# Kernel tuning notes

Measured on AMD Instinct MI355X. Metric: run time of the kernel, lower is better.

The kernel has to match this reference:

```python
import jax, jax.numpy as jnp
import numpy as np


def setup_inputs() -> dict:
    key = jax.random.key(0)
    k1, k2, k3 = jax.random.split(key, 3)
    B, C, H, W = 64, 2048, 14, 14
    M, NC = 32, 396
    x = jax.random.normal(k1, (B, C, H, W), dtype=jnp.float32)
    Wa = jax.random.normal(k2, (M, C), dtype=jnp.float32) * (1.0 / np.sqrt(C))
    ba = jnp.zeros((M,), dtype=jnp.float32)
    Wc = jax.random.normal(k3, (NC, M * C), dtype=jnp.float32) * (1.0 / np.sqrt(M * C))
    bc = jnp.zeros((NC,), dtype=jnp.float32)
    return {"x": x, "Wa": Wa, "ba": ba, "Wc": Wc, "bc": bc}


def reference(x, Wa, ba, Wc, bc):
    # x: [B, C, H, W]
    B, C, H, W = x.shape
    M = Wa.shape[0]
    # 1x1 conv == channel contraction; attention maps [B, M, H, W]
    A = jax.nn.sigmoid(jnp.einsum('bchw,mc->bmhw', x, Wa) + ba[None, :, None, None])
    # BAP: per-head attention-weighted global average pool -> [B, M, C]
    bap = jnp.einsum('bchw,bmhw->bmc', x, A) / (H * W)
    feats = bap.reshape(B, M * C)  # concat head-major, matching torch cat order
    return feats @ Wc.T + bc
```

## Files before the change

kernel.cpp:

```cpp
#include <hip/hip_runtime.h>
#include <hip/hip_bf16.h>
#include <cstdint>

#define B_N 64
#define C_N 2048
#define HW_N 196
#define HWP 224
#define M_N 32
#define NC_N 396
#define K_N 65536
#define CCH 256
#define NCH 8
#define ZSTRIDE (B_N * M_N * HW_N)

typedef __attribute__((ext_vector_type(8))) short bf16x8;
typedef __attribute__((ext_vector_type(4))) float f32x4;

__device__ inline short f2bf(float x) {
  union { float f; unsigned u; } v; v.f = x;
  unsigned r = (v.u + 0x7FFFu + ((v.u >> 16) & 1u)) >> 16;
  return (short)r;
}

__device__ inline unsigned packbf2(float lo, float hi) {
  return ((unsigned)(unsigned short)f2bf(hi) << 16) |
         (unsigned)(unsigned short)f2bf(lo);
}

__global__ __launch_bounds__(256) void k1a_partial(
    const float* __restrict__ x, const float* __restrict__ Wa,
    float* __restrict__ z) {
  __shared__ short waT[32][264];
  __shared__ short xT[208][40];
  const int t = threadIdx.x;
  const int w = t >> 6, lane = t & 63, lq = lane >> 4, ln = lane & 15;
  const int cx = blockIdx.x, b = blockIdx.y;
  const int c0 = cx * CCH;

  unsigned* xTw = (unsigned*)xT;
  if (t < 240) xTw[196 * 20 + t] = 0u;
  for (int i = t; i < 2048; i += 256) {
    int m = i >> 6, f4 = i & 63;
    float4 v = *(const float4*)(Wa + (size_t)m * C_N + c0 + f4 * 4);
    uint2 pk;
    pk.x = packbf2(v.x, v.y);
    pk.y = packbf2(v.z, v.w);
    *(uint2*)((char*)waT + m * 528 + f4 * 8) = pk;
  }

  f32x4 acc[4][2];
#pragma unroll
  for (int ti = 0; ti < 4; ++ti) {
    acc[ti][0] = (f32x4){0.f, 0.f, 0.f, 0.f};
    acc[ti][1] = (f32x4){0.f, 0.f, 0.f, 0.f};
  }

  const float* __restrict__ xb0 = x + (size_t)b * (C_N * HW_N) + (size_t)c0 * HW_N;
  const int p0 = t & 15;
  const int q0 = t >> 4;

  for (int ss = 0; ss < 8; ++ss) {
    const float* xs = xb0 + (size_t)ss * 32 * HW_N;
    {
      const float* r0 = xs + (2 * p0) * HW_N + 4 * q0;
      float4 fa0 = *(const float4*)r0;
      float4 fb0 = *(const float4*)(r0 + HW_N);
      float4 fa1 = *(const float4*)(r0 + 64);
      float4 fb1 = *(const float4*)(r0 + 64 + HW_N);
      float4 fa2 = *(const float4*)(r0 + 128);
      float4 fb2 = *(const float4*)(r0 + 128 + HW_N);
      unsigned* d0 = xTw + q0 * 80 + p0;
      d0[0]  = packbf2(fa0.x, fb0.x);
      d0[20] = packbf2(fa0.y, fb0.y);
      d0[40] = packbf2(fa0.z, fb0.z);
      d0[60] = packbf2(fa0.w, fb0.w);
      unsigned* d1 = d0 + 1280;
      d1[0]  = packbf2(fa1.x, fb1.x);
      d1[20] = packbf2(fa1.y, fb1.y);
      d1[40] = packbf2(fa1.z, fb1.z);
      d1[60] = packbf2(fa1.w, fb1.w);
      unsigned* d2 = d0 + 2560;
      d2[0]  = packbf2(fa2.x, fb2.x);
      d2[20] = packbf2(fa2.y, fb2.y);
      d2[40] = packbf2(fa2.z, fb2.z);
      d2[60] = packbf2(fa2.w, fb2.w);
      if (t < 16) {
        const float* r3 = xs + (2 * t) * HW_N + 192;
        float4 fa3 = *(const float4*)r3;
        float4 fb3 = *(const float4*)(r3 + HW_N);
        unsigned* d3 = xTw + 48 * 80 + t;
        d3[0]  = packbf2(fa3.x, fb3.x);
        d3[20] = packbf2(fa3.y, fb3.y);
        d3[40] = packbf2(fa3.z, fb3.z);
        d3[60] = packbf2(fa3.w, fb3.w);
      }
    }
    __syncthreads();
    const int kb = ss * 64 + lq * 16;
    bf16x8 af0 = *(const bf16x8*)((const char*)waT + ln * 528 + kb);
    bf16x8 af1 = *(const bf16x8*)((const char*)waT + (16 + ln) * 528 + kb);
#pragma unroll
    for (int ti = 0; ti < 4; ++ti) {
      int ht = w + ti * 4;
      if (ht < 13) {
        bf16x8 bfr = *(const bf16x8*)((const char*)xT + (ht * 16 + ln) * 80 + lq * 16);
        acc[ti][0] = __builtin_amdgcn_mfma_f32_16x16x32_bf16(af0, bfr, acc[ti][0], 0, 0, 0);
        acc[ti][1] = __builtin_amdgcn_mfma_f32_16x16x32_bf16(af1, bfr, acc[ti][1], 0, 0, 0);
      }
    }
    __syncthreads();
  }

  float* zc = z + (size_t)(cx * B_N + b) * (M_N * HW_N);
#pragma unroll
  for (int ti = 0; ti < 4; ++ti) {
    int ht = w + ti * 4;
    if (ht < 13) {
      int hw = ht * 16 + ln;
      if (hw < HW_N) {
#pragma unroll
        for (int mt = 0; mt < 2; ++mt) {
#pragma unroll
          for (int r = 0; r < 4; ++r) {
            int m = mt * 16 + lq * 4 + r;
            zc[(size_t)m * HW_N + hw] = acc[ti][mt][r];
          }
        }
      }
    }
  }
}

__global__ __launch_bounds__(256) void k1b_sig(
    const float* __restrict__ z, const float* __restrict__ ba,
    short* __restrict__ Apad) {
  int idx = blockIdx.x * 256 + threadIdx.x;
  int b = idx / (M_N * HWP);
  int r = idx - b * (M_N * HWP);
  int m = r / HWP;
  int hw = r - m * HWP;
  short out = 0;
  if (hw < HW_N) {
    float s = ba[m];
    size_t base = ((size_t)b * M_N + m) * HW_N + hw;
#pragma unroll
    for (int cx = 0; cx < NCH; ++cx)
      s += z[(size_t)cx * ZSTRIDE + base];
    out = f2bf(1.f / (1.f + __expf(-s)));
  }
  Apad[idx] = out;
}

__global__ __launch_bounds__(256) void k2_bap(
    const float* __restrict__ x, const short* __restrict__ Apad,
    short* __restrict__ featsb) {
  const int t = threadIdx.x;
  const int w = t >> 6, lane = t & 63, lq = lane >> 4, ln = lane & 15;
  const int b = blockIdx.y;
  const int c = blockIdx.x * 64 + w * 16 + ln;
  const float* __restrict__ xrow = x + (size_t)b * (C_N * HW_N) + (size_t)c * HW_N;
  const short* __restrict__ ap0 = Apad + ((size_t)b * M_N + ln) * HWP + lq * 8;
  const short* __restrict__ ap1 = ap0 + 16 * HWP;

  f32x4 d0 = {0.f, 0.f, 0.f, 0.f}, d1 = {0.f, 0.f, 0.f, 0.f};
#pragma unroll
  for (int s = 0; s < 7; ++s) {
    bf16x8 a0 = *(const bf16x8*)(ap0 + s * 32);
    bf16x8 a1 = *(const bf16x8*)(ap1 + s * 32);
    bf16x8 bfr;
    const int h = s * 32 + lq * 8;
    if (s < 6) {
      float4 b0 = *(const float4*)(xrow + h);
      float4 b1 = *(const float4*)(xrow + h + 4);
      bfr[0]=f2bf(b0.x); bfr[1]=f2bf(b0.y); bfr[2]=f2bf(b0.z); bfr[3]=f2bf(b0.w);
      bfr[4]=f2bf(b1.x); bfr[5]=f2bf(b1.y); bfr[6]=f2bf(b1.z); bfr[7]=f2bf(b1.w);
    } else {
      float4 b0 = make_float4(0.f, 0.f, 0.f, 0.f);
      if (lq == 0) b0 = *(const float4*)(xrow + h);
      bfr[0]=f2bf(b0.x); bfr[1]=f2bf(b0.y); bfr[2]=f2bf(b0.z); bfr[3]=f2bf(b0.w);
      bfr[4]=0; bfr[5]=0; bfr[6]=0; bfr[7]=0;
    }
    d0 = __builtin_amdgcn_mfma_f32_16x16x32_bf16(a0, bfr, d0, 0, 0, 0);
    d1 = __builtin_amdgcn_mfma_f32_16x16x32_bf16(a1, bfr, d1, 0, 0, 0);
  }
  const float sc = 1.f / (float)HW_N;
  short* fb = featsb + (size_t)b * K_N + c;
#pragma unroll
  for (int r = 0; r < 4; ++r) {
    int m0 = lq * 4 + r;
    fb[(size_t)m0 * C_N]        = f2bf(d0[r] * sc);
    fb[(size_t)(16 + m0) * C_N] = f2bf(d1[r] * sc);
  }
}

__global__ __launch_bounds__(256) void k3_cls(
    const short* __restrict__ featsb, const float* __restrict__ Wc,
    float* __restrict__ partial) {
  const int t = threadIdx.x;
  const int w = t >> 6, lane = t & 63, lq = lane >> 4, ln = lane & 15;
  const int n = blockIdx.x * 64 + w * 16 + ln;
  const int nc = n < NC_N ? n : NC_N - 1;
  const size_t k0 = (size_t)blockIdx.y * 512;
  const float* __restrict__ wrow = Wc + (size_t)nc * K_N + k0 + lq * 8;
  const short* __restrict__ f0 = featsb + k0 + lq * 8 + (size_t)ln * K_N;

  f32x4 acc0 = {0.f,0.f,0.f,0.f}, acc1 = {0.f,0.f,0.f,0.f};
  f32x4 acc2 = {0.f,0.f,0.f,0.f}, acc3 = {0.f,0.f,0.f,0.f};
#pragma unroll 4
  for (int s = 0; s < 16; ++s) {
    const int kk = s * 32;
    float4 w0 = *(const float4*)(wrow + kk);
    float4 w1 = *(const float4*)(wrow + kk + 4);
    bf16x8 bfr;
    bfr[0]=f2bf(w0.x); bfr[1]=f2bf(w0.y); bfr[2]=f2bf(w0.z); bfr[3]=f2bf(w0.w);
    bfr[4]=f2bf(w1.x); bfr[5]=f2bf(w1.y); bfr[6]=f2bf(w1.z); bfr[7]=f2bf(w1.w);
    bf16x8 a0 = *(const bf16x8*)(f0 + kk);
    bf16x8 a1 = *(const bf16x8*)(f0 + (size_t)16 * K_N + kk);
    bf16x8 a2 = *(const bf16x8*)(f0 + (size_t)32 * K_N + kk);
    bf16x8 a3 = *(const bf16x8*)(f0 + (size_t)48 * K_N + kk);
    acc0 = __builtin_amdgcn_mfma_f32_16x16x32_bf16(a0, bfr, acc0, 0, 0, 0);
    acc1 = __builtin_amdgcn_mfma_f32_16x16x32_bf16(a1, bfr, acc1, 0, 0, 0);
    acc2 = __builtin_amdgcn_mfma_f32_16x16x32_bf16(a2, bfr, acc2, 0, 0, 0);
    acc3 = __builtin_amdgcn_mfma_f32_16x16x32_bf16(a3, bfr, acc3, 0, 0, 0);
  }
  if (n < NC_N) {
    float* po = partial + (size_t)blockIdx.y * (B_N * NC_N) + n;
#pragma unroll
    for (int r = 0; r < 4; ++r) {
      int br = lq * 4 + r;
      po[(size_t)br * NC_N]        = acc0[r];
      po[(size_t)(16 + br) * NC_N] = acc1[r];
      po[(size_t)(32 + br) * NC_N] = acc2[r];
      po[(size_t)(48 + br) * NC_N] = acc3[r];
    }
  }
}

__global__ __launch_bounds__(256) void k4_reduce(
    const float* __restrict__ partial, const float* __restrict__ bc,
    float* __restrict__ out) {
  int idx = blockIdx.x * 256 + threadIdx.x;
  if (idx >= B_N * NC_N) return;
  int n = idx % NC_N;
  float s = bc[n];
#pragma unroll 8
  for (int kc = 0; kc < 128; ++kc) s += partial[(size_t)kc * (B_N * NC_N) + idx];
  out[idx] = s;
}

extern "C" void kernel_launch(void* const* d_in, const int* in_sizes, int n_in,
                              void* d_out, int out_size, void* d_ws, size_t ws_size,
                              hipStream_t stream) {
  const float* x  = (const float*)d_in[0];
  const float* Wa = (const float*)d_in[1];
  const float* ba = (const float*)d_in[2];
  const float* Wc = (const float*)d_in[3];
  const float* bc = (const float*)d_in[4];
  float* out = (float*)d_out;

  char* wsb = (char*)d_ws;
  short* Apad    = (short*)(wsb);
  short* featsb  = (short*)(wsb + (1u  << 20));
  float* partial = (float*)(wsb + (10u << 20));
  float* zbuf    = (float*)(wsb + (10u << 20));
  (void)ws_size; (void)in_sizes; (void)n_in; (void)out_size;

  hipLaunchKernelGGL(k1a_partial, dim3(NCH, B_N), dim3(256), 0, stream,
                     x, Wa, zbuf);
  hipLaunchKernelGGL(k1b_sig, dim3(1792), dim3(256), 0, stream,
                     zbuf, ba, Apad);
  hipLaunchKernelGGL(k2_bap, dim3(32, 64), dim3(256), 0, stream,
                     x, Apad, featsb);
  hipLaunchKernelGGL(k3_cls, dim3(7, 128), dim3(256), 0, stream,
                     featsb, Wc, partial);
  hipLaunchKernelGGL(k4_reduce, dim3(99), dim3(256), 0, stream,
                     partial, bc, out);
}
```

Before: 284.5 us.

## Store feats in MFMA-fragment-tiled layout and prefetch classifier operands

The BAP kernel now writes pooled features into a tiled layout that matches the MFMA A-fragment order. Each wave in the classifier then reads one contiguous 1 KB chunk per fragment instead of 16 rows strided by 64K elements. The classifier loop is also software-pipelined, loading the next step's Wc and feature fragments before issuing the current MFMAs. The aim is better coalescing and hidden load latency in the dominant GEMV-like stage, at the cost of more registers and scattered writes in the BAP kernel.

```diff
diff --git a/kernel.cpp b/kernel.cpp
--- a/kernel.cpp
+++ b/kernel.cpp
@@ -184,12 +184,15 @@
     d1 = __builtin_amdgcn_mfma_f32_16x16x32_bf16(a1, bfr, d1, 0, 0, 0);
   }
   const float sc = 1.f / (float)HW_N;
-  short* fb = featsb + (size_t)b * K_N + c;
+  const int bt = b >> 4, bl = b & 15;
+  const int lq2 = (c >> 3) & 3, j = c & 7;
+  const int cs5 = c >> 5;
+  short* fb = featsb + ((size_t)bt * 64 + (size_t)lq2 * 16 + bl) * 8 + j;
 #pragma unroll
   for (int r = 0; r < 4; ++r) {
     int m0 = lq * 4 + r;
-    fb[(size_t)m0 * C_N]        = f2bf(d0[r] * sc);
-    fb[(size_t)(16 + m0) * C_N] = f2bf(d1[r] * sc);
+    fb[(size_t)(m0 * 64 + cs5) * 2048]        = f2bf(d0[r] * sc);
+    fb[(size_t)((16 + m0) * 64 + cs5) * 2048] = f2bf(d1[r] * sc);
   }
 }
 
@@ -200,28 +203,45 @@
   const int w = t >> 6, lane = t & 63, lq = lane >> 4, ln = lane & 15;
   const int n = blockIdx.x * 64 + w * 16 + ln;
   const int nc = n < NC_N ? n : NC_N - 1;
-  const size_t k0 = (size_t)blockIdx.y * 512;
+  const int kc = blockIdx.y;
+  const size_t k0 = (size_t)kc * 512;
   const float* __restrict__ wrow = Wc + (size_t)nc * K_N + k0 + lq * 8;
-  const short* __restrict__ f0 = featsb + k0 + lq * 8 + (size_t)ln * K_N;
+  const short* __restrict__ fb = featsb + (size_t)(kc * 16) * 2048 + lane * 8;
 
   f32x4 acc0 = {0.f,0.f,0.f,0.f}, acc1 = {0.f,0.f,0.f,0.f};
   f32x4 acc2 = {0.f,0.f,0.f,0.f}, acc3 = {0.f,0.f,0.f,0.f};
-#pragma unroll 4
+
+  float4 cw0 = *(const float4*)(wrow);
+  float4 cw1 = *(const float4*)(wrow + 4);
+  bf16x8 ca0 = *(const bf16x8*)(fb);
+  bf16x8 ca1 = *(const bf16x8*)(fb + 512);
+  bf16x8 ca2 = *(const bf16x8*)(fb + 1024);
+  bf16x8 ca3 = *(const bf16x8*)(fb + 1536);
+
+#pragma unroll
   for (int s = 0; s < 16; ++s) {
-    const int kk = s * 32;
-    float4 w0 = *(const float4*)(wrow + kk);
-    float4 w1 = *(const float4*)(wrow + kk + 4);
+    float4 nw0, nw1; bf16x8 na0, na1, na2, na3;
+    if (s < 15) {
+      const float* wn = wrow + (s + 1) * 32;
+      nw0 = *(const float4*)(wn);
+      nw1 = *(const float4*)(wn + 4);
+      const short* fs = fb + (size_t)(s + 1) * 2048;
+      na0 = *(const bf16x8*)(fs);
+      na1 = *(const bf16x8*)(fs + 512);
+      na2 = *(const bf16x8*)(fs + 1024);
+      na3 = *(const bf16x8*)(fs + 1536);
+    }
     bf16x8 bfr;
-    bfr[0]=f2bf(w0.x); bfr[1]=f2bf(w0.y); bfr[2]=f2bf(w0.z); bfr[3]=f2bf(w0.w);
-    bfr[4]=f2bf(w1.x); bfr[5]=f2bf(w1.y); bfr[6]=f2bf(w1.z); bfr[7]=f2bf(w1.w);
-    bf16x8 a0 = *(const bf16x8*)(f0 + kk);
-    bf16x8 a1 = *(const bf16x8*)(f0 + (size_t)16 * K_N + kk);
-    bf16x8 a2 = *(const bf16x8*)(f0 + (size_t)32 * K_N + kk);
-    bf16x8 a3 = *(const bf16x8*)(f0 + (size_t)48 * K_N + kk);
-    acc0 = __builtin_amdgcn_mfma_f32_16x16x32_bf16(a0, bfr, acc0, 0, 0, 0);
-    acc1 = __builtin_amdgcn_mfma_f32_16x16x32_bf16(a1, bfr, acc1, 0, 0, 0);
-    acc2 = __builtin_amdgcn_mfma_f32_16x16x32_bf16(a2, bfr, acc2, 0, 0, 0);
-    acc3 = __builtin_amdgcn_mfma_f32_16x16x32_bf16(a3, bfr, acc3, 0, 0, 0);
+    bfr[0]=f2bf(cw0.x); bfr[1]=f2bf(cw0.y); bfr[2]=f2bf(cw0.z); bfr[3]=f2bf(cw0.w);
+    bfr[4]=f2bf(cw1.x); bfr[5]=f2bf(cw1.y); bfr[6]=f2bf(cw1.z); bfr[7]=f2bf(cw1.w);
+    acc0 = __builtin_amdgcn_mfma_f32_16x16x32_bf16(ca0, bfr, acc0, 0, 0, 0);
+    acc1 = __builtin_amdgcn_mfma_f32_16x16x32_bf16(ca1, bfr, acc1, 0, 0, 0);
+    acc2 = __builtin_amdgcn_mfma_f32_16x16x32_bf16(ca2, bfr, acc2, 0, 0, 0);
+    acc3 = __builtin_amdgcn_mfma_f32_16x16x32_bf16(ca3, bfr, acc3, 0, 0, 0);
+    if (s < 15) {
+      cw0 = nw0; cw1 = nw1;
+      ca0 = na0; ca1 = na1; ca2 = na2; ca3 = na3;
+    }
   }
   if (n < NC_N) {
     float* po = partial + (size_t)blockIdx.y * (B_N * NC_N) + n;
```

After: 279.4 us. No clear change (-1.8%).
